# Kernel optimization log

Measured on AMD Instinct MI355X. Metric: run time of the kernel, lower is better.

Reference implementation:

```python
import jax, jax.numpy as jnp
import numpy as np

DIM = 768
NUM_HEADS = 12
HEAD_DIM = DIM // NUM_HEADS
SCALE = HEAD_DIM ** -0.5
ELEV_SCALE = 1000.0


def setup_inputs() -> dict:
    key = jax.random.key(0)
    ks = jax.random.split(key, 6)
    B, N = 2, 2048
    x = jax.random.normal(ks[0], (B, N, DIM), dtype=jnp.float32)
    # elevation in meters, roughly 0..3000 m
    elevation_patches = jax.random.uniform(ks[1], (B, N), dtype=jnp.float32) * 3000.0
    # torch nn.Linear weights are [out, in]; y = x @ W.T + b
    w_qkv = jax.random.normal(ks[2], (3 * DIM, DIM), dtype=jnp.float32) * (DIM ** -0.5)
    w_proj = jax.random.normal(ks[3], (DIM, DIM), dtype=jnp.float32) * (DIM ** -0.5)
    b_proj = jax.random.normal(ks[4], (DIM,), dtype=jnp.float32) * 0.02
    alpha = jnp.ones((1,), dtype=jnp.float32)
    return {"x": x, "elevation_patches": elevation_patches,
            "w_qkv": w_qkv, "w_proj": w_proj, "b_proj": b_proj, "alpha": alpha}


def _elevation_bias(elev, alpha):
    # elev: [B, N] -> bias [B, N, N]; penalize uphill (elev_j > elev_i)
    diff = (elev[:, None, :] - elev[:, :, None]) / ELEV_SCALE  # [B, N, N]
    bias = -alpha[0] * jax.nn.relu(diff)
    return jnp.clip(bias, -10.0, 0.0)


def reference(x, elevation_patches, w_qkv, w_proj, b_proj, alpha):
    B, N, D = x.shape
    H, Hd = NUM_HEADS, HEAD_DIM
    qkv = x @ w_qkv.T                                   # [B, N, 3D]
    qkv = qkv.reshape(B, N, 3, H, Hd)
    q = jnp.transpose(qkv[:, :, 0], (0, 2, 1, 3))       # [B, H, N, Hd]
    k = jnp.transpose(qkv[:, :, 1], (0, 2, 1, 3))
    v = jnp.transpose(qkv[:, :, 2], (0, 2, 1, 3))
    scores = jnp.einsum('bhnd,bhmd->bhnm', q, k) * SCALE  # [B, H, N, N]
    bias = _elevation_bias(elevation_patches, alpha)       # [B, N, N]
    scores = scores + bias[:, None, :, :]
    attn = jax.nn.softmax(scores, axis=-1)
    out = jnp.einsum('bhnm,bhmd->bhnd', attn, v)           # [B, H, N, Hd]
    out = jnp.transpose(out, (0, 2, 1, 3)).reshape(B, N, D)
    return out @ w_proj.T + b_proj
```

## Files before the change

### kernel.cpp

```cpp
#include <hip/hip_runtime.h>


typedef __attribute__((ext_vector_type(8))) short bf16x8;
typedef __attribute__((ext_vector_type(4))) float f32x4;
typedef __attribute__((ext_vector_type(16))) float f32x16;

__device__ __forceinline__ unsigned short f2bf(float f) {
  unsigned int u = __builtin_bit_cast(unsigned int, f);
  u += 0x7fffu + ((u >> 16) & 1u);
  return (unsigned short)(u >> 16);
}

__device__ __forceinline__ unsigned cvtpk(float lo, float hi) {
  unsigned r;
  asm("v_cvt_pk_bf16_f32 %0, %1, %2" : "=v"(r) : "v"(lo), "v"(hi));
  return r;
}

__device__ __forceinline__ float exp2v(float x) {
  float r;
  asm("v_exp_f32 %0, %1" : "=v"(r) : "v"(x));
  return r;
}

__device__ __forceinline__ int sw8(int row) {
  return ((row ^ (row >> 3)) & 7) << 3;
}

__device__ __forceinline__ void gload16(const unsigned short* g, unsigned short* l) {
  __builtin_amdgcn_global_load_lds(
      (const __attribute__((address_space(1))) unsigned int*)g,
      (__attribute__((address_space(3))) unsigned int*)l, 16, 0, 0);
}

__global__ __launch_bounds__(256)
void cvt2_kernel(const float* __restrict__ a, unsigned short* __restrict__ ao, int na8,
                 const float* __restrict__ b, unsigned short* __restrict__ bo, int nb8) {
  int i = blockIdx.x * 256 + threadIdx.x;
  const float* src; unsigned short* dst;
  if (i < na8) { src = a; dst = ao; }
  else {
    i -= na8;
    if (i >= nb8) return;
    src = b; dst = bo;
  }
  const float4 f0 = ((const float4*)src)[i * 2];
  const float4 f1 = ((const float4*)src)[i * 2 + 1];
  uint4 v;
  v.x = cvtpk(f0.x, f0.y);
  v.y = cvtpk(f0.z, f0.w);
  v.z = cvtpk(f1.x, f1.y);
  v.w = cvtpk(f1.z, f1.w);
  ((uint4*)dst)[i] = v;
}

__global__ __launch_bounds__(256)
void gemm_a32_kernel(const float* __restrict__ Ap,
                     const unsigned short* __restrict__ Bp,
                     unsigned short* __restrict__ Cp, int M, int N, int K) {
  __shared__ __align__(16) unsigned short lds_a[2][128 * 32];
  __shared__ __align__(16) unsigned short lds_b[2][128 * 32];
  const int t = threadIdx.x;
  const int l = t & 63;
  const int w = t >> 6;
  const int wr = w >> 1, wc = w & 1;
  const int brow = blockIdx.x * 128;
  const int bcol = blockIdx.y * 128;
  const int l15 = l & 15, l4 = l >> 4;

  const int srow = t >> 2;
  const int scol = (t & 3) * 8;
  const float* ga = Ap + (size_t)(brow + srow) * K + scol;
  const unsigned short* gb = Bp + (size_t)(bcol + srow) * K + scol;

  f32x4 acc[4][4] = {};
  const int nk = K >> 5;

  float4 fa[4];
  {
    fa[0] = *(const float4*)ga;
    fa[1] = *(const float4*)(ga + 4);
    fa[2] = *(const float4*)(ga + (size_t)64 * K);
    fa[3] = *(const float4*)(ga + (size_t)64 * K + 4);
    unsigned short* lb = lds_b[0] + w * 512;
    gload16(gb, lb);
    gload16(gb + (size_t)64 * K, lb + 2048);
    uint4 u0, u1;
    u0.x = cvtpk(fa[0].x, fa[0].y); u0.y = cvtpk(fa[0].z, fa[0].w);
    u0.z = cvtpk(fa[1].x, fa[1].y); u0.w = cvtpk(fa[1].z, fa[1].w);
    u1.x = cvtpk(fa[2].x, fa[2].y); u1.y = cvtpk(fa[2].z, fa[2].w);
    u1.z = cvtpk(fa[3].x, fa[3].y); u1.w = cvtpk(fa[3].z, fa[3].w);
    *(uint4*)&lds_a[0][srow * 32 + scol] = u0;
    *(uint4*)&lds_a[0][(srow + 64) * 32 + scol] = u1;
  }
  __syncthreads();

  int buf = 0;
  for (int kt = 0; kt < nk; ++kt) {
    const bool more = kt + 1 < nk;
    if (more) {
      const size_t ko = (size_t)(kt + 1) * 32;
      fa[0] = *(const float4*)(ga + ko);
      fa[1] = *(const float4*)(ga + ko + 4);
      fa[2] = *(const float4*)(ga + ko + (size_t)64 * K);
      fa[3] = *(const float4*)(ga + ko + (size_t)64 * K + 4);
      unsigned short* lb = lds_b[buf ^ 1] + w * 512;
      gload16(gb + ko, lb);
      gload16(gb + ko + (size_t)64 * K, lb + 2048);
    }
    bf16x8 af[4], bfr[4];
#pragma unroll
    for (int i = 0; i < 4; ++i) {
      af[i]  = *(const bf16x8*)&lds_a[buf][(wr * 64 + i * 16 + l15) * 32 + l4 * 8];
      bfr[i] = *(const bf16x8*)&lds_b[buf][(wc * 64 + i * 16 + l15) * 32 + l4 * 8];
    }
#pragma unroll
    for (int i = 0; i < 4; ++i)
#pragma unroll
      for (int j = 0; j < 4; ++j)
        acc[i][j] = __builtin_amdgcn_mfma_f32_16x16x32_bf16(af[i], bfr[j], acc[i][j], 0, 0, 0);
    if (more) {
      uint4 u0, u1;
      u0.x = cvtpk(fa[0].x, fa[0].y); u0.y = cvtpk(fa[0].z, fa[0].w);
      u0.z = cvtpk(fa[1].x, fa[1].y); u0.w = cvtpk(fa[1].z, fa[1].w);
      u1.x = cvtpk(fa[2].x, fa[2].y); u1.y = cvtpk(fa[2].z, fa[2].w);
      u1.z = cvtpk(fa[3].x, fa[3].y); u1.w = cvtpk(fa[3].z, fa[3].w);
      *(uint4*)&lds_a[buf ^ 1][srow * 32 + scol] = u0;
      *(uint4*)&lds_a[buf ^ 1][(srow + 64) * 32 + scol] = u1;
    }
    __syncthreads();
    buf ^= 1;
  }

#pragma unroll
  for (int i = 0; i < 4; ++i)
#pragma unroll
    for (int j = 0; j < 4; ++j)
#pragma unroll
      for (int r = 0; r < 4; ++r) {
        const int row = brow + wr * 64 + i * 16 + l4 * 4 + r;
        const int col = bcol + wc * 64 + j * 16 + l15;
        Cp[(size_t)row * N + col] = f2bf(acc[i][j][r]);
      }
}

__global__ __launch_bounds__(256)
void gemm2_kernel(const unsigned short* __restrict__ Ap,
                  const unsigned short* __restrict__ Bp,
                  const float* __restrict__ bias, float* __restrict__ Cp,
                  int M, int N, int K) {
  __shared__ __align__(16) unsigned short lds_a[2][64 * 32];
  __shared__ __align__(16) unsigned short lds_b[2][128 * 32];
  const int t = threadIdx.x;
  const int l = t & 63;
  const int w = t >> 6;
  const int wr = w >> 1, wc = w & 1;
  const int brow = blockIdx.x * 64;
  const int bcol = blockIdx.y * 128;
  const int l15 = l & 15, l4 = l >> 4;

  const int srow = t >> 2;
  const int scol = (t & 3) * 8;
  const unsigned short* ga = Ap + (size_t)(brow + srow) * K + scol;
  const unsigned short* gb = Bp + (size_t)(bcol + srow) * K + scol;

  f32x4 acc[2][4] = {};
  const int nk = K >> 5;

  {
    gload16(ga, lds_a[0] + w * 512);
    unsigned short* lb = lds_b[0] + w * 512;
    gload16(gb, lb);
    gload16(gb + (size_t)64 * K, lb + 2048);
  }
  __syncthreads();

  int buf = 0;
  for (int kt = 0; kt < nk; ++kt) {
    if (kt + 1 < nk) {
      const size_t ko = (size_t)(kt + 1) * 32;
      gload16(ga + ko, lds_a[buf ^ 1] + w * 512);
      unsigned short* lb = lds_b[buf ^ 1] + w * 512;
      gload16(gb + ko, lb);
      gload16(gb + ko + (size_t)64 * K, lb + 2048);
    }
    bf16x8 af[2], bfr[4];
#pragma unroll
    for (int i = 0; i < 2; ++i)
      af[i] = *(const bf16x8*)&lds_a[buf][(wr * 32 + i * 16 + l15) * 32 + l4 * 8];
#pragma unroll
    for (int j = 0; j < 4; ++j)
      bfr[j] = *(const bf16x8*)&lds_b[buf][(wc * 64 + j * 16 + l15) * 32 + l4 * 8];
#pragma unroll
    for (int i = 0; i < 2; ++i)
#pragma unroll
      for (int j = 0; j < 4; ++j)
        acc[i][j] = __builtin_amdgcn_mfma_f32_16x16x32_bf16(af[i], bfr[j], acc[i][j], 0, 0, 0);
    __syncthreads();
    buf ^= 1;
  }

#pragma unroll
  for (int i = 0; i < 2; ++i)
#pragma unroll
    for (int j = 0; j < 4; ++j)
#pragma unroll
      for (int r = 0; r < 4; ++r) {
        const int row = brow + wr * 32 + i * 16 + l4 * 4 + r;
        const int col = bcol + wc * 64 + j * 16 + l15;
        Cp[(size_t)row * N + col] = acc[i][j][r] + bias[col];
      }
}

__global__ __launch_bounds__(256)
void attn_kernel(const unsigned short* __restrict__ qkv,
                 const float* __restrict__ elev,
                 const float* __restrict__ alpha_p,
                 unsigned short* __restrict__ aout) {
  __shared__ __align__(16) unsigned short lds_k[2][64 * 64];
  __shared__ __align__(16) unsigned short lds_vt[2][64 * 64];
  __shared__ __align__(16) float lds_ej[2][64];

  const int t = threadIdx.x;
  const int l = t & 63;
  const int w = t >> 6;
  const int l31 = l & 31;
  const int h = l >> 5;
  const int b = blockIdx.x / 12, hd = blockIdx.x % 12;
  const int q0 = blockIdx.y * 128 + w * 32;

  const float cE = fmaxf(alpha_p[0], 0.f) * (1.4426950408889634f * 1e-3f);
  const float c1 = 0.18033688011112042f;

  const size_t rs = 2304;
  const unsigned short* qbase = qkv + ((size_t)b * 2048) * rs + hd * 64;
  const unsigned short* kbase = qbase + 768;
  const unsigned short* vbase = qbase + 1536;

  bf16x8 qa[4];
  {
    const unsigned short* qp = qbase + (size_t)(q0 + l31) * rs + h * 8;
#pragma unroll
    for (int ks = 0; ks < 4; ++ks) qa[ks] = *(const bf16x8*)(qp + ks * 16);
  }
  const float eiv = elev[(size_t)b * 2048 + q0 + l31] * cE;

  uint4 onesu; onesu.x = onesu.y = onesu.z = onesu.w = 0x3F803F80u;
  const bf16x8 onesf = __builtin_bit_cast(bf16x8, onesu);

  f32x16 o[2] = {};
  f32x16 ps = {};

  const int sr = t >> 3;
  const int sc = (t & 7) * 8;

  uint4 rk[2], rv[2];
  float evn = 0.f;

#pragma unroll
  for (int p = 0; p < 2; ++p) {
    const int r = p * 32 + sr;
    rk[p] = *(const uint4*)(kbase + (size_t)r * rs + sc);
    rv[p] = *(const uint4*)(vbase + (size_t)r * rs + sc);
  }
  if (t < 64) evn = elev[(size_t)b * 2048 + t];
#pragma unroll
  for (int p = 0; p < 2; ++p) {
    const int r = p * 32 + sr;
    *(uint4*)&lds_k[0][r * 64 + (sc ^ sw8(r))] = rk[p];
    union { uint4 u; unsigned short s[8]; } vu; vu.u = rv[p];
#pragma unroll
    for (int j = 0; j < 8; ++j) {
      const int d = sc + j;
      lds_vt[0][d * 64 + (r ^ sw8(d))] = vu.s[j];
    }
  }
  if (t < 64) lds_ej[0][t] = evn * cE;
  __syncthreads();

  for (int it = 0; it < 32; ++it) {
    const int cur = it & 1;
    const bool more = it < 31;
    if (more) {
      const int kv1 = (it + 1) * 64;
#pragma unroll
      for (int p = 0; p < 2; ++p) {
        const int r = kv1 + p * 32 + sr;
        rk[p] = *(const uint4*)(kbase + (size_t)r * rs + sc);
        rv[p] = *(const uint4*)(vbase + (size_t)r * rs + sc);
      }
      if (t < 64) evn = elev[(size_t)b * 2048 + kv1 + t];
    }

    f32x16 st[2] = {};
    __builtin_amdgcn_s_setprio(1);
#pragma unroll
    for (int kst = 0; kst < 4; ++kst) {
      const int col = kst * 16 + h * 8;
#pragma unroll
      for (int mb = 0; mb < 2; ++mb) {
        const int row = mb * 32 + l31;
        bf16x8 kf = *(const bf16x8*)&lds_k[cur][row * 64 + (col ^ sw8(row))];
        st[mb] = __builtin_amdgcn_mfma_f32_32x32x16_bf16(kf, qa[kst], st[mb], 0, 0, 0);
      }
    }
    __builtin_amdgcn_s_setprio(0);

    bf16x8 pa[4];
#pragma unroll
    for (int mb = 0; mb < 2; ++mb) {
      float p16[16];
#pragma unroll
      for (int rr = 0; rr < 4; ++rr) {
        const float4 ejq = *(const float4*)&lds_ej[cur][mb * 32 + rr * 8 + h * 4];
#pragma unroll
        for (int jl = 0; jl < 4; ++jl) {
          const int r = rr * 4 + jl;
          const float bm = __builtin_amdgcn_fmed3f(ejq[jl] - eiv, 0.f, 14.4269504f);
          p16[r] = exp2v(__builtin_fmaf(st[mb][r], c1, -bm));
        }
      }
#pragma unroll
      for (int ks2 = 0; ks2 < 2; ++ks2) {
        unsigned u0 = cvtpk(p16[ks2 * 8 + 0], p16[ks2 * 8 + 1]);
        unsigned u1 = cvtpk(p16[ks2 * 8 + 2], p16[ks2 * 8 + 3]);
        unsigned v0 = cvtpk(p16[ks2 * 8 + 4], p16[ks2 * 8 + 5]);
        unsigned v1 = cvtpk(p16[ks2 * 8 + 6], p16[ks2 * 8 + 7]);
        asm volatile("v_permlane32_swap_b32 %0, %1" : "+v"(u0), "+v"(v0));
        asm volatile("v_permlane32_swap_b32 %0, %1" : "+v"(u1), "+v"(v1));
        uint4 fr; fr.x = u0; fr.y = u1; fr.z = v0; fr.w = v1;
        pa[mb * 2 + ks2] = __builtin_bit_cast(bf16x8, fr);
      }
    }

    __builtin_amdgcn_s_setprio(1);
#pragma unroll
    for (int ks = 0; ks < 4; ++ks) {
      const int col = ks * 16 + h * 8;
#pragma unroll
      for (int nb = 0; nb < 2; ++nb) {
        const int row = nb * 32 + l31;
        bf16x8 vf = *(const bf16x8*)&lds_vt[cur][row * 64 + (col ^ sw8(row))];
        o[nb] = __builtin_amdgcn_mfma_f32_32x32x16_bf16(pa[ks], vf, o[nb], 0, 0, 0);
      }
      ps = __builtin_amdgcn_mfma_f32_32x32x16_bf16(pa[ks], onesf, ps, 0, 0, 0);
    }
    __builtin_amdgcn_s_setprio(0);

    if (more) {
      const int nxt = cur ^ 1;
#pragma unroll
      for (int p = 0; p < 2; ++p) {
        const int r = p * 32 + sr;
        *(uint4*)&lds_k[nxt][r * 64 + (sc ^ sw8(r))] = rk[p];
        union { uint4 u; unsigned short s[8]; } vu; vu.u = rv[p];
#pragma unroll
        for (int j = 0; j < 8; ++j) {
          const int d = sc + j;
          lds_vt[nxt][d * 64 + (r ^ sw8(d))] = vu.s[j];
        }
      }
      if (t < 64) lds_ej[nxt][t] = evn * cE;
      __syncthreads();
    }
  }

  float inv[16];
#pragma unroll
  for (int r = 0; r < 16; ++r) inv[r] = 1.0f / ps[r];
#pragma unroll
  for (int nb = 0; nb < 2; ++nb) {
    const int col = hd * 64 + nb * 32 + l31;
#pragma unroll
    for (int rr = 0; rr < 4; ++rr)
#pragma unroll
      for (int jl = 0; jl < 4; ++jl) {
        const int r = rr * 4 + jl;
        const int q = q0 + rr * 8 + h * 4 + jl;
        aout[((size_t)b * 2048 + q) * 768 + col] = f2bf(o[nb][r] * inv[r]);
      }
  }
}

extern "C" void kernel_launch(void* const* d_in, const int* in_sizes, int n_in,
                              void* d_out, int out_size, void* d_ws, size_t ws_size,
                              hipStream_t stream) {
  const float* x      = (const float*)d_in[0];
  const float* elev   = (const float*)d_in[1];
  const float* w_qkv  = (const float*)d_in[2];
  const float* w_proj = (const float*)d_in[3];
  const float* b_proj = (const float*)d_in[4];
  const float* alpha  = (const float*)d_in[5];
  float* out = (float*)d_out;

  unsigned short* qkvb   = (unsigned short*)d_ws;
  unsigned short* aob    = qkvb + (size_t)4096 * 2304;
  unsigned short* wqkvb  = aob + (size_t)4096 * 768;
  unsigned short* wprojb = wqkvb + (size_t)2304 * 768;

  cvt2_kernel<<<1152, 256, 0, stream>>>(w_qkv, wqkvb, 2304 * 768 / 8,
                                        w_proj, wprojb, 768 * 768 / 8);

  gemm_a32_kernel<<<dim3(32, 18), 256, 0, stream>>>(
      x, wqkvb, qkvb, 4096, 2304, 768);

  attn_kernel<<<dim3(24, 16), 256, 0, stream>>>(qkvb, elev, alpha, aob);

  gemm2_kernel<<<dim3(64, 6), 256, 0, stream>>>(
      aob, wprojb, b_proj, out, 4096, 768, 768);
}
```

Baseline: 117.7 us.

## Split attention KV loop across two wave groups and remap QKV GEMM blocks per XCD

The attention kernel now runs 512 threads per block. Two groups of four waves each process alternating 64-row KV tiles over 16 steps and merge their partial outputs and row sums through LDS at the end. This doubles the waves per block so the serial KV loop is shortened and more latency can be hidden, at the cost of twice the LDS and an extra reduction and barrier. Separately, the QKV GEMM remaps block IDs so that neighbouring row tiles land on the same XCD, which is meant to improve L2 reuse of the weight tiles.

```diff
diff --git a/kernel.cpp b/kernel.cpp
--- a/kernel.cpp
+++ b/kernel.cpp
@@ -64,8 +64,11 @@
   const int l = t & 63;
   const int w = t >> 6;
   const int wr = w >> 1, wc = w & 1;
-  const int brow = blockIdx.x * 128;
-  const int bcol = blockIdx.y * 128;
+  const int bid = blockIdx.x + gridDim.x * blockIdx.y;
+  const int xcd = bid & 7;
+  const int idx = bid >> 3;
+  const int brow = (xcd * 4 + (idx & 3)) * 128;
+  const int bcol = (idx >> 2) * 128;
   const int l15 = l & 15, l4 = l >> 4;
 
   const int srow = t >> 2;
@@ -212,22 +215,24 @@
       }
 }
 
-__global__ __launch_bounds__(256)
+__global__ __launch_bounds__(512)
 void attn_kernel(const unsigned short* __restrict__ qkv,
                  const float* __restrict__ elev,
                  const float* __restrict__ alpha_p,
                  unsigned short* __restrict__ aout) {
-  __shared__ __align__(16) unsigned short lds_k[2][64 * 64];
-  __shared__ __align__(16) unsigned short lds_vt[2][64 * 64];
-  __shared__ __align__(16) float lds_ej[2][64];
+  __shared__ __align__(16) unsigned short lds_k[2][2][64 * 64];
+  __shared__ __align__(16) unsigned short lds_vt[2][2][64 * 64];
+  __shared__ __align__(16) float lds_ej[2][2][64];
 
   const int t = threadIdx.x;
   const int l = t & 63;
   const int w = t >> 6;
+  const int wq = w & 3;
+  const int par = w >> 2;
   const int l31 = l & 31;
   const int h = l >> 5;
   const int b = blockIdx.x / 12, hd = blockIdx.x % 12;
-  const int q0 = blockIdx.y * 128 + w * 32;
+  const int q0 = blockIdx.y * 128 + wq * 32;
 
   const float cE = fmaxf(alpha_p[0], 0.f) * (1.4426950408889634f * 1e-3f);
   const float c1 = 0.18033688011112042f;
@@ -256,40 +261,38 @@
 
   uint4 rk[2], rv[2];
   float evn = 0.f;
+  const int ejp = t >> 6;
 
 #pragma unroll
   for (int p = 0; p < 2; ++p) {
-    const int r = p * 32 + sr;
-    rk[p] = *(const uint4*)(kbase + (size_t)r * rs + sc);
-    rv[p] = *(const uint4*)(vbase + (size_t)r * rs + sc);
-  }
-  if (t < 64) evn = elev[(size_t)b * 2048 + t];
+    rk[p] = *(const uint4*)(kbase + (size_t)(p * 64 + sr) * rs + sc);
+    rv[p] = *(const uint4*)(vbase + (size_t)(p * 64 + sr) * rs + sc);
+  }
+  if (t < 128) evn = elev[(size_t)b * 2048 + ejp * 64 + (t & 63)];
 #pragma unroll
   for (int p = 0; p < 2; ++p) {
-    const int r = p * 32 + sr;
-    *(uint4*)&lds_k[0][r * 64 + (sc ^ sw8(r))] = rk[p];
+    *(uint4*)&lds_k[p][0][sr * 64 + (sc ^ sw8(sr))] = rk[p];
     union { uint4 u; unsigned short s[8]; } vu; vu.u = rv[p];
 #pragma unroll
     for (int j = 0; j < 8; ++j) {
       const int d = sc + j;
-      lds_vt[0][d * 64 + (r ^ sw8(d))] = vu.s[j];
-    }
-  }
-  if (t < 64) lds_ej[0][t] = evn * cE;
+      lds_vt[p][0][d * 64 + (sr ^ sw8(d))] = vu.s[j];
+    }
+  }
+  if (t < 128) lds_ej[ejp][0][t & 63] = evn * cE;
   __syncthreads();
 
-  for (int it = 0; it < 32; ++it) {
-    const int cur = it & 1;
-    const bool more = it < 31;
+  for (int s = 0; s < 16; ++s) {
+    const int cur = s & 1;
+    const bool more = s < 15;
     if (more) {
-      const int kv1 = (it + 1) * 64;
+      const int kvn = (2 * (s + 1)) * 64;
 #pragma unroll
       for (int p = 0; p < 2; ++p) {
-        const int r = kv1 + p * 32 + sr;
-        rk[p] = *(const uint4*)(kbase + (size_t)r * rs + sc);
-        rv[p] = *(const uint4*)(vbase + (size_t)r * rs + sc);
-      }
-      if (t < 64) evn = elev[(size_t)b * 2048 + kv1 + t];
+        rk[p] = *(const uint4*)(kbase + (size_t)(kvn + p * 64 + sr) * rs + sc);
+        rv[p] = *(const uint4*)(vbase + (size_t)(kvn + p * 64 + sr) * rs + sc);
+      }
+      if (t < 128) evn = elev[(size_t)b * 2048 + kvn + ejp * 64 + (t & 63)];
     }
 
     f32x16 st[2] = {};
@@ -300,7 +303,7 @@
 #pragma unroll
       for (int mb = 0; mb < 2; ++mb) {
         const int row = mb * 32 + l31;
-        bf16x8 kf = *(const bf16x8*)&lds_k[cur][row * 64 + (col ^ sw8(row))];
+        bf16x8 kf = *(const bf16x8*)&lds_k[par][cur][row * 64 + (col ^ sw8(row))];
         st[mb] = __builtin_amdgcn_mfma_f32_32x32x16_bf16(kf, qa[kst], st[mb], 0, 0, 0);
       }
     }
@@ -312,7 +315,7 @@
       float p16[16];
 #pragma unroll
       for (int rr = 0; rr < 4; ++rr) {
-        const float4 ejq = *(const float4*)&lds_ej[cur][mb * 32 + rr * 8 + h * 4];
+        const float4 ejq = *(const float4*)&lds_ej[par][cur][mb * 32 + rr * 8 + h * 4];
 #pragma unroll
         for (int jl = 0; jl < 4; ++jl) {
           const int r = rr * 4 + jl;
@@ -340,7 +343,7 @@
 #pragma unroll
       for (int nb = 0; nb < 2; ++nb) {
         const int row = nb * 32 + l31;
-        bf16x8 vf = *(const bf16x8*)&lds_vt[cur][row * 64 + (col ^ sw8(row))];
+        bf16x8 vf = *(const bf16x8*)&lds_vt[par][cur][row * 64 + (col ^ sw8(row))];
         o[nb] = __builtin_amdgcn_mfma_f32_32x32x16_bf16(pa[ks], vf, o[nb], 0, 0, 0);
       }
       ps = __builtin_amdgcn_mfma_f32_32x32x16_bf16(pa[ks], onesf, ps, 0, 0, 0);
@@ -351,34 +354,51 @@
       const int nxt = cur ^ 1;
 #pragma unroll
       for (int p = 0; p < 2; ++p) {
-        const int r = p * 32 + sr;
-        *(uint4*)&lds_k[nxt][r * 64 + (sc ^ sw8(r))] = rk[p];
+        *(uint4*)&lds_k[p][nxt][sr * 64 + (sc ^ sw8(sr))] = rk[p];
         union { uint4 u; unsigned short s[8]; } vu; vu.u = rv[p];
 #pragma unroll
         for (int j = 0; j < 8; ++j) {
           const int d = sc + j;
-          lds_vt[nxt][d * 64 + (r ^ sw8(d))] = vu.s[j];
+          lds_vt[p][nxt][d * 64 + (sr ^ sw8(d))] = vu.s[j];
         }
       }
-      if (t < 64) lds_ej[nxt][t] = evn * cE;
-      __syncthreads();
-    }
-  }
-
-  float inv[16];
-#pragma unroll
-  for (int r = 0; r < 16; ++r) inv[r] = 1.0f / ps[r];
-#pragma unroll
-  for (int nb = 0; nb < 2; ++nb) {
-    const int col = hd * 64 + nb * 32 + l31;
-#pragma unroll
-    for (int rr = 0; rr < 4; ++rr)
-#pragma unroll
-      for (int jl = 0; jl < 4; ++jl) {
-        const int r = rr * 4 + jl;
-        const int q = q0 + rr * 8 + h * 4 + jl;
-        aout[((size_t)b * 2048 + q) * 768 + col] = f2bf(o[nb][r] * inv[r]);
-      }
+      if (t < 128) lds_ej[ejp][nxt][t & 63] = evn * cE;
+    }
+    __syncthreads();
+  }
+
+  float* xO = (float*)lds_k;
+  float* xP = (float*)lds_vt;
+  const int cbase = (wq * 64 + l) * 16;
+  if (par == 1) {
+#pragma unroll
+    for (int r = 0; r < 16; ++r) {
+      xO[cbase + r] = o[0][r];
+      xO[4096 + cbase + r] = o[1][r];
+      xP[cbase + r] = ps[r];
+    }
+  }
+  __syncthreads();
+  if (par == 0) {
+    float inv[16];
+#pragma unroll
+    for (int r = 0; r < 16; ++r) {
+      o[0][r] += xO[cbase + r];
+      o[1][r] += xO[4096 + cbase + r];
+      inv[r] = 1.0f / (ps[r] + xP[cbase + r]);
+    }
+#pragma unroll
+    for (int nb = 0; nb < 2; ++nb) {
+      const int col = hd * 64 + nb * 32 + l31;
+#pragma unroll
+      for (int rr = 0; rr < 4; ++rr)
+#pragma unroll
+        for (int jl = 0; jl < 4; ++jl) {
+          const int r = rr * 4 + jl;
+          const int q = q0 + rr * 8 + h * 4 + jl;
+          aout[((size_t)b * 2048 + q) * 768 + col] = f2bf(o[nb][r] * inv[r]);
+        }
+    }
   }
 }
 
@@ -404,7 +424,7 @@
   gemm_a32_kernel<<<dim3(32, 18), 256, 0, stream>>>(
       x, wqkvb, qkvb, 4096, 2304, 768);
 
-  attn_kernel<<<dim3(24, 16), 256, 0, stream>>>(qkvb, elev, alpha, aob);
+  attn_kernel<<<dim3(24, 16), 512, 0, stream>>>(qkvb, elev, alpha, aob);
 
   gemm2_kernel<<<dim3(64, 6), 256, 0, stream>>>(
       aob, wprojb, b_proj, out, 4096, 768, 768);
```

After: 119.9 us. About the same (+1.8%).
